# Kernel optimization log

Hardware: AMD Instinct MI355X
Metric: run time of the kernel (lower is better)

The kernel has to match this reference:

```python
import jax, jax.numpy as jnp
import numpy as np
import math

N_HEADS = 16
DIM = 1024
D_HEAD = DIM // N_HEADS
BS, QLEN = 2, 2048


def setup_inputs() -> dict:
    key = jax.random.key(0)
    ks = jax.random.split(key, 10)
    s = 0.02
    return {
        "input": jax.random.normal(ks[0], (BS, QLEN, DIM), dtype=jnp.float32),
        "mask": jnp.ones((BS, QLEN), dtype=jnp.int32),
        "q_w": jax.random.normal(ks[1], (DIM, DIM), dtype=jnp.float32) * s,
        "q_b": jax.random.normal(ks[2], (DIM,), dtype=jnp.float32) * s,
        "k_w": jax.random.normal(ks[3], (DIM, DIM), dtype=jnp.float32) * s,
        "k_b": jax.random.normal(ks[4], (DIM,), dtype=jnp.float32) * s,
        "v_w": jax.random.normal(ks[5], (DIM, DIM), dtype=jnp.float32) * s,
        "v_b": jax.random.normal(ks[6], (DIM,), dtype=jnp.float32) * s,
        "o_w": jax.random.normal(ks[7], (DIM, DIM), dtype=jnp.float32) * s,
        "o_b": jax.random.normal(ks[8], (DIM,), dtype=jnp.float32) * s,
    }


def _shape(x, bs):
    # (bs, len, dim) -> (bs, heads, len, d_head)
    return x.reshape(bs, -1, N_HEADS, D_HEAD).transpose(0, 2, 1, 3)


def reference(input, mask, q_w, q_b, k_w, k_b, v_w, v_b, o_w, o_b):
    bs, qlen, dim = input.shape
    # projections (torch Linear: x @ W^T + b)
    q = _shape(input @ q_w.T + q_b, bs)
    k = _shape(input @ k_w.T + k_b, bs)
    v = _shape(input @ v_w.T + v_b, bs)
    q = q / math.sqrt(D_HEAD)
    # scores: (bs, heads, qlen, klen)
    scores = jnp.einsum("bhqd,bhkd->bhqk", q, k)
    pad = (mask == 0)[:, None, None, :]  # (bs,1,1,klen)
    scores = jnp.where(pad, -jnp.inf, scores)
    weights = jax.nn.softmax(scores.astype(jnp.float32), axis=-1).astype(scores.dtype)
    # dropout p=0.0 (eval) -> identity
    context = jnp.einsum("bhqk,bhkd->bhqd", weights, v)
    context = context.transpose(0, 2, 1, 3).reshape(bs, qlen, dim)
    return context @ o_w.T + o_b
```

## Files before the change

kernel.cpp:

```cpp
#include <hip/hip_runtime.h>


#define BS    2
#define QLEN  2048
#define DIM   1024
#define NH    16
#define DH    64
#define MTOK  (BS * QLEN)

#define QSCALE 0.18033688011112042f

typedef __attribute__((ext_vector_type(8))) short short8;
typedef __attribute__((ext_vector_type(4))) float float4_t;
typedef __attribute__((ext_vector_type(4))) int   int4_t;

__device__ __forceinline__ ushort f2bf(float f) {
    unsigned u = __float_as_uint(f);
    return (ushort)((u + 0x7fffu + ((u >> 16) & 1u)) >> 16);
}
__device__ __forceinline__ short8 pack8(float4 a0, float4 a1) {
    short8 r;
    r[0] = (short)f2bf(a0.x); r[1] = (short)f2bf(a0.y);
    r[2] = (short)f2bf(a0.z); r[3] = (short)f2bf(a0.w);
    r[4] = (short)f2bf(a1.x); r[5] = (short)f2bf(a1.y);
    r[6] = (short)f2bf(a1.z); r[7] = (short)f2bf(a1.w);
    return r;
}

__device__ __forceinline__ void glds16(const void* g, void* l) {
    __builtin_amdgcn_global_load_lds(
        (const __attribute__((address_space(1))) unsigned int*)g,
        (__attribute__((address_space(3))) unsigned int*)l, 16, 0, 0);
}

__global__ __launch_bounds__(256) void conv_all(
    const float* __restrict__ x,  const float* __restrict__ qw,
    const float* __restrict__ kw, const float* __restrict__ vw,
    const float* __restrict__ ow,
    ushort* __restrict__ Xbf, ushort* __restrict__ Wbf)
{
    const int blk = blockIdx.x;
    const float* s; ushort* d; size_t base;
    if (blk < 4096)      { s = x;  d = Xbf;             base = (size_t)blk * 1024; }
    else if (blk < 5120) { s = qw; d = Wbf;             base = (size_t)(blk - 4096) * 1024; }
    else if (blk < 6144) { s = kw; d = Wbf + 1048576;   base = (size_t)(blk - 5120) * 1024; }
    else if (blk < 7168) { s = vw; d = Wbf + 2097152;   base = (size_t)(blk - 6144) * 1024; }
    else                 { s = ow; d = Wbf + 3145728;   base = (size_t)(blk - 7168) * 1024; }
    const size_t i = base + threadIdx.x * 4;
    float4 v = *(const float4*)(s + i);
    ushort4 o;
    o.x = f2bf(v.x); o.y = f2bf(v.y); o.z = f2bf(v.z); o.w = f2bf(v.w);
    *(ushort4*)(d + i) = o;
}

__global__ __launch_bounds__(256) void transpose_v(
    const ushort* __restrict__ Vrow, ushort* __restrict__ Vt)
{
    __shared__ ushort T[64][72];
    const int tid  = threadIdx.x;
    const int tile = blockIdx.x;
    const int bh   = blockIdx.y;
    const int b = bh >> 4, h = bh & 15;

    #pragma unroll
    for (int rep = 0; rep < 2; ++rep) {
        int ch = tid + rep * 256;
        int tok = ch >> 3, seg = ch & 7;
        uint4 v = *(const uint4*)(Vrow + (size_t)(b * QLEN + tile * 64 + tok) * DIM
                                        + h * DH + seg * 8);
        *(uint4*)&T[tok][seg * 8] = v;
    }
    __syncthreads();
    #pragma unroll
    for (int rep = 0; rep < 2; ++rep) {
        int ch = tid + rep * 256;
        int dim = ch >> 3, tseg = ch & 7;
        ushort t0 = T[tseg * 8 + 0][dim], t1 = T[tseg * 8 + 1][dim];
        ushort t2 = T[tseg * 8 + 2][dim], t3 = T[tseg * 8 + 3][dim];
        ushort t4 = T[tseg * 8 + 4][dim], t5 = T[tseg * 8 + 5][dim];
        ushort t6 = T[tseg * 8 + 6][dim], t7 = T[tseg * 8 + 7][dim];
        uint4 o;
        o.x = (unsigned)t0 | ((unsigned)t1 << 16);
        o.y = (unsigned)t2 | ((unsigned)t3 << 16);
        o.z = (unsigned)t4 | ((unsigned)t5 << 16);
        o.w = (unsigned)t6 | ((unsigned)t7 << 16);
        *(uint4*)(Vt + (size_t)bh * DH * QLEN + (size_t)dim * QLEN
                      + tile * 64 + tseg * 8) = o;
    }
}

__global__ __launch_bounds__(256) void gemm_qkv(
    const ushort* __restrict__ A, const ushort* __restrict__ Bw,
    const float* __restrict__ bias0, const float* __restrict__ bias1,
    const float* __restrict__ bias2,
    ushort* __restrict__ outQ, ushort* __restrict__ outK, ushort* __restrict__ outVt)
{
    __shared__ ushort As[2][128 * 32];
    __shared__ ushort Bs[2][128 * 32];
    const int tid  = threadIdx.x;
    const int w    = tid >> 6;
    const int lane = tid & 63;
    const int r15  = lane & 15;
    const int quad = lane >> 4;
    const int xcd = blockIdx.x & 7;
    const int lid = blockIdx.x >> 3;
    const int brow = (xcd & 3) * 8  + (lid & 7);
    const int bcol = (xcd >> 2) * 12 + (lid >> 3);
    const int wrow = (w >> 1) * 64;
    const int wcol = (w & 1) * 64;
    const int K = DIM;

    float4_t acc[4][4];
    #pragma unroll
    for (int i = 0; i < 4; ++i)
        #pragma unroll
        for (int j = 0; j < 4; ++j)
            acc[i][j] = (float4_t){0.f, 0.f, 0.f, 0.f};

    int chS[2];
    const ushort* gaS[2];
    const ushort* gbS[2];
    #pragma unroll
    for (int rep = 0; rep < 2; ++rep) {
        const int ch  = w * 128 + rep * 64 + lane;
        const int row = ch >> 2;
        const int g   = (ch & 3) ^ ((row >> 1) & 3);
        chS[rep] = ch;
        gaS[rep] = A  + (size_t)(brow * 128 + row) * K + g * 8;
        gbS[rep] = Bw + (size_t)(bcol * 128 + row) * K + g * 8;
    }
    const int ph = (quad ^ ((r15 >> 1) & 3)) * 8;

    #pragma unroll
    for (int rep = 0; rep < 2; ++rep) {
        glds16(gaS[rep], &As[0][chS[rep] * 8]);
        glds16(gbS[rep], &Bs[0][chS[rep] * 8]);
    }
    __syncthreads();

    int p = 0;
    for (int k0 = 0; k0 < K; k0 += 32) {
        if (k0 + 32 < K) {
            #pragma unroll
            for (int rep = 0; rep < 2; ++rep) {
                glds16(gaS[rep] + k0 + 32, &As[p ^ 1][chS[rep] * 8]);
                glds16(gbS[rep] + k0 + 32, &Bs[p ^ 1][chS[rep] * 8]);
            }
        }
        short8 af[4], bf[4];
        #pragma unroll
        for (int ms = 0; ms < 4; ++ms)
            af[ms] = *(const short8*)&As[p][(wrow + ms * 16 + r15) * 32 + ph];
        #pragma unroll
        for (int ns = 0; ns < 4; ++ns)
            bf[ns] = *(const short8*)&Bs[p][(wcol + ns * 16 + r15) * 32 + ph];
        #pragma unroll
        for (int ms = 0; ms < 4; ++ms)
            #pragma unroll
            for (int ns = 0; ns < 4; ++ns)
                acc[ms][ns] = __builtin_amdgcn_mfma_f32_16x16x32_bf16(
                    af[ms], bf[ns], acc[ms][ns], 0, 0, 0);
        __syncthreads();
        p ^= 1;
    }

    #pragma unroll
    for (int ms = 0; ms < 4; ++ms) {
        const int rowg = brow * 128 + wrow + ms * 16 + quad * 4;
        #pragma unroll
        for (int ns = 0; ns < 4; ++ns) {
            const int colg = bcol * 128 + wcol + ns * 16 + r15;
            if (colg < 1024) {
                const float bb = bias0[colg];
                #pragma unroll
                for (int r = 0; r < 4; ++r)
                    outQ[(size_t)(rowg + r) * 1024 + colg] =
                        f2bf((acc[ms][ns][r] + bb) * QSCALE);
            } else if (colg < 2048) {
                const float bb = bias1[colg - 1024];
                #pragma unroll
                for (int r = 0; r < 4; ++r)
                    outK[(size_t)(rowg + r) * 1024 + (colg - 1024)] =
                        f2bf(acc[ms][ns][r] + bb);
            } else {
                const int vcol = colg - 2048;
                const int hh = vcol >> 6, dd = vcol & 63;
                const float bb = bias2[vcol];
                const int bidx = rowg >> 11;
                const int tloc = rowg & 2047;
                ushort4 o4;
                o4.x = f2bf(acc[ms][ns][0] + bb);
                o4.y = f2bf(acc[ms][ns][1] + bb);
                o4.z = f2bf(acc[ms][ns][2] + bb);
                o4.w = f2bf(acc[ms][ns][3] + bb);
                *(ushort4*)&outVt[((size_t)(bidx * 16 + hh) * 64 + dd) * QLEN + tloc] = o4;
            }
        }
    }
}

__global__ __launch_bounds__(256) void gemm_o(
    const ushort* __restrict__ A, const ushort* __restrict__ Bw,
    const float* __restrict__ bias, float* __restrict__ Out)
{
    __shared__ ushort As[2][128 * 64];
    __shared__ ushort Bs[2][64 * 64];
    const int tid  = threadIdx.x;
    const int w    = tid >> 6;
    const int lane = tid & 63;
    const int r15  = lane & 15;
    const int quad = lane >> 4;
    const int xcd = blockIdx.x & 7;
    const int lid = blockIdx.x >> 3;
    const int brow = (xcd & 3) * 8 + (lid & 7);
    const int bcol = (xcd >> 2) * 8 + (lid >> 3);
    const int wrow = w * 32;
    const int K = DIM;

    float4_t acc[2][4];
    #pragma unroll
    for (int i = 0; i < 2; ++i)
        #pragma unroll
        for (int j = 0; j < 4; ++j)
            acc[i][j] = (float4_t){0.f, 0.f, 0.f, 0.f};

    int chA[4];  const ushort* gaS[4];
    #pragma unroll
    for (int rep = 0; rep < 4; ++rep) {
        const int ch  = w * 256 + rep * 64 + lane;
        const int row = ch >> 3;
        const int g   = (ch & 7) ^ (row & 7);
        chA[rep] = ch;
        gaS[rep] = A + (size_t)(brow * 128 + row) * K + g * 8;
    }
    int chB[2];  const ushort* gbS[2];
    #pragma unroll
    for (int rep = 0; rep < 2; ++rep) {
        const int ch  = w * 128 + rep * 64 + lane;
        const int row = ch >> 3;
        const int g   = (ch & 7) ^ (row & 7);
        chB[rep] = ch;
        gbS[rep] = Bw + (size_t)(bcol * 64 + row) * K + g * 8;
    }
    const int xg = r15 & 7;

    #pragma unroll
    for (int rep = 0; rep < 4; ++rep)
        glds16(gaS[rep], &As[0][chA[rep] * 8]);
    #pragma unroll
    for (int rep = 0; rep < 2; ++rep)
        glds16(gbS[rep], &Bs[0][chB[rep] * 8]);
    __syncthreads();

    int p = 0;
    for (int k0 = 0; k0 < K; k0 += 64) {
        if (k0 + 64 < K) {
            #pragma unroll
            for (int rep = 0; rep < 4; ++rep)
                glds16(gaS[rep] + k0 + 64, &As[p ^ 1][chA[rep] * 8]);
            #pragma unroll
            for (int rep = 0; rep < 2; ++rep)
                glds16(gbS[rep] + k0 + 64, &Bs[p ^ 1][chB[rep] * 8]);
        }
        #pragma unroll
        for (int hh = 0; hh < 2; ++hh) {
            const int ph = ((hh * 4 + quad) ^ xg) * 8;
            short8 af[2], bf[4];
            #pragma unroll
            for (int ms = 0; ms < 2; ++ms)
                af[ms] = *(const short8*)&As[p][(wrow + ms * 16 + r15) * 64 + ph];
            #pragma unroll
            for (int ns = 0; ns < 4; ++ns)
                bf[ns] = *(const short8*)&Bs[p][(ns * 16 + r15) * 64 + ph];
            #pragma unroll
            for (int ms = 0; ms < 2; ++ms)
                #pragma unroll
                for (int ns = 0; ns < 4; ++ns)
                    acc[ms][ns] = __builtin_amdgcn_mfma_f32_16x16x32_bf16(
                        af[ms], bf[ns], acc[ms][ns], 0, 0, 0);
        }
        __syncthreads();
        p ^= 1;
    }

    #pragma unroll
    for (int ms = 0; ms < 2; ++ms) {
        const int rowg = brow * 128 + wrow + ms * 16 + quad * 4;
        #pragma unroll
        for (int ns = 0; ns < 4; ++ns) {
            const int colg = bcol * 64 + ns * 16 + r15;
            const float bb = bias[colg];
            #pragma unroll
            for (int r = 0; r < 4; ++r)
                Out[(size_t)(rowg + r) * 1024 + colg] = acc[ms][ns][r] + bb;
        }
    }
}

__global__ __launch_bounds__(256) void gemm_f32in_bf16out(
    const float* __restrict__ X, const float* __restrict__ W,
    const float* __restrict__ B, ushort* __restrict__ Out,
    int M, int N, int K, float scale)
{
    const int lane = threadIdx.x & 63;
    const int wid  = (blockIdx.x * blockDim.x + threadIdx.x) >> 6;
    const int tilesN = N >> 4;
    const int tm = wid / tilesN;
    const int tn = wid - tm * tilesN;
    const int r15  = lane & 15;
    const int quad = lane >> 4;

    const float* xp = X + (size_t)(tm * 16 + r15) * K + quad * 8;
    const float* wp = W + (size_t)(tn * 16 + r15) * K + quad * 8;

    float4_t acc = {0.f, 0.f, 0.f, 0.f};
    for (int k0 = 0; k0 < K; k0 += 32) {
        float4 a0 = *(const float4*)(xp + k0);
        float4 a1 = *(const float4*)(xp + k0 + 4);
        float4 b0 = *(const float4*)(wp + k0);
        float4 b1 = *(const float4*)(wp + k0 + 4);
        acc = __builtin_amdgcn_mfma_f32_16x16x32_bf16(pack8(a0, a1), pack8(b0, b1), acc, 0, 0, 0);
    }
    const int col  = tn * 16 + r15;
    const float bias = B[col];
    const int row0 = tm * 16 + quad * 4;
    #pragma unroll
    for (int r = 0; r < 4; ++r)
        Out[(size_t)(row0 + r) * N + col] = f2bf((acc[r] + bias) * scale);
}

__global__ __launch_bounds__(256) void gemm_bf16in_f32out(
    const ushort* __restrict__ X, const float* __restrict__ W,
    const float* __restrict__ B, float* __restrict__ Out,
    int M, int N, int K)
{
    const int lane = threadIdx.x & 63;
    const int wid  = (blockIdx.x * blockDim.x + threadIdx.x) >> 6;
    const int tilesN = N >> 4;
    const int tm = wid / tilesN;
    const int tn = wid - tm * tilesN;
    const int r15  = lane & 15;
    const int quad = lane >> 4;

    const ushort* xp = X + (size_t)(tm * 16 + r15) * K + quad * 8;
    const float*  wp = W + (size_t)(tn * 16 + r15) * K + quad * 8;

    float4_t acc = {0.f, 0.f, 0.f, 0.f};
    for (int k0 = 0; k0 < K; k0 += 32) {
        short8 a = *(const short8*)(xp + k0);
        float4 b0 = *(const float4*)(wp + k0);
        float4 b1 = *(const float4*)(wp + k0 + 4);
        acc = __builtin_amdgcn_mfma_f32_16x16x32_bf16(a, pack8(b0, b1), acc, 0, 0, 0);
    }
    const int col  = tn * 16 + r15;
    const float bias = B[col];
    const int row0 = tm * 16 + quad * 4;
    #pragma unroll
    for (int r = 0; r < 4; ++r)
        Out[(size_t)(row0 + r) * N + col] = acc[r] + bias;
}

__global__ __launch_bounds__(256, 2) void flash_attn(
    const ushort* __restrict__ Qb, const ushort* __restrict__ Kb,
    const ushort* __restrict__ Vt, const int* __restrict__ mask,
    ushort* __restrict__ Cb)
{
    __shared__ __align__(16) ushort Ks[2][64][64];
    __shared__ __align__(16) ushort Vs[2][64][64];
    __shared__ __align__(16) float  Mb[QLEN];

    const int tid  = threadIdx.x;
    const int w    = tid >> 6;
    const int lane = tid & 63;
    const int r15  = lane & 15;
    const int quad = lane >> 4;
    const int bh = blockIdx.y;
    const int b = bh >> 4, h = bh & 15;

    {
        const int4* m4 = (const int4*)(mask + b * QLEN);
        #pragma unroll
        for (int rep = 0; rep < 2; ++rep) {
            const int idx = tid + rep * 256;
            int4 mv = m4[idx];
            float4 o;
            o.x = mv.x ? 0.f : -INFINITY;
            o.y = mv.y ? 0.f : -INFINITY;
            o.z = mv.z ? 0.f : -INFINITY;
            o.w = mv.w ? 0.f : -INFINITY;
            *(float4*)&Mb[idx * 4] = o;
        }
    }

    const int qbase = blockIdx.x * 128 + w * 32;
    const ushort* qp = Qb + (size_t)(b * QLEN + qbase + r15) * DIM + h * DH + quad * 8;
    short8 qf[2][2];
    qf[0][0] = *(const short8*)(qp);
    qf[0][1] = *(const short8*)(qp + 32);
    qf[1][0] = *(const short8*)(qp + 16 * DIM);
    qf[1][1] = *(const short8*)(qp + 16 * DIM + 32);

    const ushort* kg = Kb + (size_t)b * QLEN * DIM + h * DH;
    const ushort* vg = Vt + (size_t)bh * DH * QLEN;

    int cc0, cc1;
    const ushort* gk[2];
    const ushort* gv[2];
    {
        #pragma unroll
        for (int rep = 0; rep < 2; ++rep) {
            const int c   = (w * 2 + rep) * 64 + lane;
            const int row = c >> 3, slot = c & 7;
            const int sg  = slot ^ (row & 7);
            const int r5  = row & 31;
            const int tok = (row & 32) | (((r5 >> 3) & 1) << 4) | (((r5 >> 2) & 1) << 3)
                          | (((r5 >> 4) & 1) << 2) | (r5 & 3);
            if (rep == 0) cc0 = c; else cc1 = c;
            gk[rep] = kg + (size_t)tok * DIM  + sg * 8;
            gv[rep] = vg + (size_t)row * QLEN + sg * 8;
        }
    }

    const int xq = (quad ^ (r15 & 7)) << 3;

    float4_t o[2][4];
    float4_t ol[2];
    #pragma unroll
    for (int rg = 0; rg < 2; ++rg) {
        ol[rg] = (float4_t){0.f, 0.f, 0.f, 0.f};
        #pragma unroll
        for (int ds = 0; ds < 4; ++ds)
            o[rg][ds] = (float4_t){0.f, 0.f, 0.f, 0.f};
    }
    short8 ones8;
    #pragma unroll
    for (int i = 0; i < 8; ++i) ones8[i] = (short)0x3F80;

    int pkA[4][2][2], pkB[4][2][2];

#define STAGE_K(BUF, KT) do {                                                 \
    glds16(gk[0] + (size_t)(KT) * DIM, (ushort*)Ks[BUF] + cc0 * 8);           \
    glds16(gk[1] + (size_t)(KT) * DIM, (ushort*)Ks[BUF] + cc1 * 8);           \
} while (0)

#define STAGE_V(BUF, KT) do {                                                 \
    glds16(gv[0] + (KT), (ushort*)Vs[BUF] + cc0 * 8);                         \
    glds16(gv[1] + (KT), (ushort*)Vs[BUF] + cc1 * 8);                         \
} while (0)

#define S_PHASE(KBUF, KT, PK) do {                                            \
    _Pragma("unroll")                                                         \
    for (int ks = 0; ks < 4; ++ks) {                                          \
        const ushort* krow = &Ks[KBUF][ks * 16 + r15][0];                     \
        short8 kf0 = *(const short8*)(krow + xq);                             \
        short8 kf1 = *(const short8*)(krow + (xq ^ 32));                      \
        const float4 mb = *(const float4*)&Mb[(KT) + ((ks >> 1) << 5)         \
                                              + (quad << 3) + ((ks & 1) << 2)]; \
        _Pragma("unroll")                                                     \
        for (int rg = 0; rg < 2; ++rg) {                                      \
            float4_t s = {0.f, 0.f, 0.f, 0.f};                                \
            s = __builtin_amdgcn_mfma_f32_16x16x32_bf16(kf0, qf[rg][0], s, 0, 0, 0); \
            s = __builtin_amdgcn_mfma_f32_16x16x32_bf16(kf1, qf[rg][1], s, 0, 0, 0); \
            unsigned u0 = __float_as_uint(__builtin_amdgcn_exp2f(s[0] + mb.x)); \
            unsigned u1 = __float_as_uint(__builtin_amdgcn_exp2f(s[1] + mb.y)); \
            unsigned u2 = __float_as_uint(__builtin_amdgcn_exp2f(s[2] + mb.z)); \
            unsigned u3 = __float_as_uint(__builtin_amdgcn_exp2f(s[3] + mb.w)); \
            PK[ks][rg][0] = __builtin_amdgcn_perm(u1, u0, 0x07060302);        \
            PK[ks][rg][1] = __builtin_amdgcn_perm(u3, u2, 0x07060302);        \
        }                                                                     \
    }                                                                         \
} while (0)

#define PV_PHASE(VBUF, PK) do {                                               \
    __builtin_amdgcn_s_setprio(1);                                            \
    _Pragma("unroll")                                                         \
    for (int ck = 0; ck < 2; ++ck) {                                          \
        short8 vf[4];                                                         \
        _Pragma("unroll")                                                     \
        for (int ds = 0; ds < 4; ++ds)                                        \
            vf[ds] = *(const short8*)(&Vs[VBUF][ds * 16 + r15][0] + (xq ^ (ck << 5))); \
        _Pragma("unroll")                                                     \
        for (int rg = 0; rg < 2; ++rg) {                                      \
            int4_t pfi = { PK[2 * ck][rg][0], PK[2 * ck][rg][1],              \
                           PK[2 * ck + 1][rg][0], PK[2 * ck + 1][rg][1] };    \
            short8 pf = __builtin_bit_cast(short8, pfi);                      \
            _Pragma("unroll")                                                 \
            for (int ds = 0; ds < 4; ++ds)                                    \
                o[rg][ds] = __builtin_amdgcn_mfma_f32_16x16x32_bf16(          \
                    pf, vf[ds], o[rg][ds], 0, 0, 0);                          \
            ol[rg] = __builtin_amdgcn_mfma_f32_16x16x32_bf16(                 \
                pf, ones8, ol[rg], 0, 0, 0);                                  \
        }                                                                     \
    }                                                                         \
    __builtin_amdgcn_s_setprio(0);                                            \
} while (0)

    STAGE_K(0, 0); STAGE_V(0, 0); STAGE_K(1, 64);
    __syncthreads();
    S_PHASE(0, 0, pkA);
    __syncthreads();

    for (int kb = 0; kb < 1856; kb += 128) {
        STAGE_V(1, kb + 64); STAGE_K(0, kb + 128);
        S_PHASE(1, kb + 64, pkB);
        PV_PHASE(0, pkA);
        __syncthreads();
        STAGE_V(0, kb + 128); STAGE_K(1, kb + 192);
        S_PHASE(0, kb + 128, pkA);
        PV_PHASE(1, pkB);
        __syncthreads();
    }

    STAGE_V(1, 1984);
    S_PHASE(1, 1984, pkB);
    PV_PHASE(0, pkA);
    __syncthreads();
    PV_PHASE(1, pkB);

#undef STAGE_K
#undef STAGE_V
#undef S_PHASE
#undef PV_PHASE

    #pragma unroll
    for (int rg = 0; rg < 2; ++rg) {
        #pragma unroll
        for (int r = 0; r < 4; ++r) {
            const float ir = 1.f / fmaxf(ol[rg][r], 1e-30f);
            const size_t rb = (size_t)(b * QLEN + qbase + rg * 16 + quad * 4 + r) * DIM
                              + h * DH;
            Cb[rb +  0 + r15] = f2bf(o[rg][0][r] * ir);
            Cb[rb + 16 + r15] = f2bf(o[rg][1][r] * ir);
            Cb[rb + 32 + r15] = f2bf(o[rg][2][r] * ir);
            Cb[rb + 48 + r15] = f2bf(o[rg][3][r] * ir);
        }
    }
}

extern "C" void kernel_launch(void* const* d_in, const int* in_sizes, int n_in,
                              void* d_out, int out_size, void* d_ws, size_t ws_size,
                              hipStream_t stream)
{
    const float* x    = (const float*)d_in[0];
    const int*   mask = (const int*)d_in[1];
    const float* q_w  = (const float*)d_in[2];
    const float* q_b  = (const float*)d_in[3];
    const float* k_w  = (const float*)d_in[4];
    const float* k_b  = (const float*)d_in[5];
    const float* v_w  = (const float*)d_in[6];
    const float* v_b  = (const float*)d_in[7];
    const float* o_w  = (const float*)d_in[8];
    const float* o_b  = (const float*)d_in[9];
    float* out = (float*)d_out;

    const size_t SEG = (size_t)MTOK * DIM;
    ushort* Qbf = (ushort*)d_out;
    ushort* Xbf = Qbf + SEG;
    ushort* Kb  = (ushort*)d_ws;
    ushort* Cb  = Kb + SEG;
    ushort* Vt  = Cb + SEG;
    ushort* Wbf = Vt + SEG;

    const bool big = ws_size >= (size_t)32 * 1024 * 1024;

    if (big) {
        conv_all<<<8192, 256, 0, stream>>>(x, q_w, k_w, v_w, o_w, Xbf, Wbf);
        gemm_qkv<<<(MTOK / 128) * (3072 / 128), 256, 0, stream>>>(
            Xbf, Wbf, q_b, k_b, v_b, Qbf, Kb, Vt);
        flash_attn<<<dim3(QLEN / 128, BS * NH), 256, 0, stream>>>(Qbf, Kb, Vt, mask, Cb);
        gemm_o<<<(MTOK / 128) * (DIM / 64), 256, 0, stream>>>(
            Cb, Wbf + 3 * (size_t)(DIM * DIM), o_b, out);
    } else {
        const int tiles   = (MTOK / 16) * (DIM / 16);
        const int gblocks = tiles / 4;
        gemm_f32in_bf16out<<<gblocks, 256, 0, stream>>>(x, q_w, q_b, Qbf, MTOK, DIM, DIM, QSCALE);
        gemm_f32in_bf16out<<<gblocks, 256, 0, stream>>>(x, k_w, k_b, Kb,  MTOK, DIM, DIM, 1.0f);
        gemm_f32in_bf16out<<<gblocks, 256, 0, stream>>>(x, v_w, v_b, Cb,  MTOK, DIM, DIM, 1.0f);
        transpose_v<<<dim3(QLEN / 64, BS * NH), 256, 0, stream>>>(Cb, Vt);
        flash_attn<<<dim3(QLEN / 128, BS * NH), 256, 0, stream>>>(Qbf, Kb, Vt, mask, Cb);
        gemm_bf16in_f32out<<<tiles / 4, 256, 0, stream>>>(Cb, o_w, o_b, out, MTOK, DIM, DIM);
    }
}
```

Measured before the change: 193.4 us.

## Double K/V tile depth to 128 keys per stage and read mask from global

The flash-attention kernel now stages 128 keys per pipeline step instead of 64, which halves the number of __syncthreads barriers and loop iterations. The shared-memory mask buffer is removed; each S phase loads the int mask directly from global and folds it into the MFMA accumulator init. In exchange, LDS use doubles to about 64KB per block and the P-fragment registers double, which risks lower occupancy under launch_bounds(256,2) and more register pressure.

```diff
diff --git a/kernel.cpp b/kernel.cpp
--- a/kernel.cpp
+++ b/kernel.cpp
@@ -365,9 +365,8 @@
     const ushort* __restrict__ Vt, const int* __restrict__ mask,
     ushort* __restrict__ Cb)
 {
-    __shared__ __align__(16) ushort Ks[2][64][64];
-    __shared__ __align__(16) ushort Vs[2][64][64];
-    __shared__ __align__(16) float  Mb[QLEN];
+    __shared__ __align__(16) ushort Ks[2][2][64][64];
+    __shared__ __align__(16) ushort Vs[2][2][64][64];
 
     const int tid  = threadIdx.x;
     const int w    = tid >> 6;
@@ -377,21 +376,6 @@
     const int bh = blockIdx.y;
     const int b = bh >> 4, h = bh & 15;
 
-    {
-        const int4* m4 = (const int4*)(mask + b * QLEN);
-        #pragma unroll
-        for (int rep = 0; rep < 2; ++rep) {
-            const int idx = tid + rep * 256;
-            int4 mv = m4[idx];
-            float4 o;
-            o.x = mv.x ? 0.f : -INFINITY;
-            o.y = mv.y ? 0.f : -INFINITY;
-            o.z = mv.z ? 0.f : -INFINITY;
-            o.w = mv.w ? 0.f : -INFINITY;
-            *(float4*)&Mb[idx * 4] = o;
-        }
-    }
-
     const int qbase = blockIdx.x * 128 + w * 32;
     const ushort* qp = Qb + (size_t)(b * QLEN + qbase + r15) * DIM + h * DH + quad * 8;
     short8 qf[2][2];
@@ -402,23 +386,21 @@
 
     const ushort* kg = Kb + (size_t)b * QLEN * DIM + h * DH;
     const ushort* vg = Vt + (size_t)bh * DH * QLEN;
-
-    int cc0, cc1;
-    const ushort* gk[2];
-    const ushort* gv[2];
-    {
-        #pragma unroll
-        for (int rep = 0; rep < 2; ++rep) {
-            const int c   = (w * 2 + rep) * 64 + lane;
-            const int row = c >> 3, slot = c & 7;
-            const int sg  = slot ^ (row & 7);
-            const int r5  = row & 31;
-            const int tok = (row & 32) | (((r5 >> 3) & 1) << 4) | (((r5 >> 2) & 1) << 3)
-                          | (((r5 >> 4) & 1) << 2) | (r5 & 3);
-            if (rep == 0) cc0 = c; else cc1 = c;
-            gk[rep] = kg + (size_t)tok * DIM  + sg * 8;
-            gv[rep] = vg + (size_t)row * QLEN + sg * 8;
-        }
+    const int*    mg = mask + b * QLEN;
+
+    int kOff[4], vOff[4];
+    #pragma unroll
+    for (int rep = 0; rep < 4; ++rep) {
+        const int c    = rep * 256 + tid;
+        const int sub  = c >> 9;
+        const int r    = (c >> 3) & 63;
+        const int slot = c & 7;
+        const int sg   = slot ^ (r & 7);
+        const int r5   = r & 31;
+        const int tokl = (r & 32) | (((r5 >> 3) & 1) << 4) | (((r5 >> 2) & 1) << 3)
+                       | (((r5 >> 4) & 1) << 2) | (r5 & 3);
+        kOff[rep] = (sub * 64 + tokl) * DIM + sg * 8;
+        vOff[rep] = r * QLEN + sub * 64 + sg * 8;
     }
 
     const int xq = (quad ^ (r15 & 7)) << 3;
@@ -436,53 +418,68 @@
     #pragma unroll
     for (int i = 0; i < 8; ++i) ones8[i] = (short)0x3F80;
 
-    int pkA[4][2][2], pkB[4][2][2];
-
-#define STAGE_K(BUF, KT) do {                                                 \
-    glds16(gk[0] + (size_t)(KT) * DIM, (ushort*)Ks[BUF] + cc0 * 8);           \
-    glds16(gk[1] + (size_t)(KT) * DIM, (ushort*)Ks[BUF] + cc1 * 8);           \
+    int pkA[2][4][2][2], pkB[2][4][2][2];
+
+#define STAGE_K(BUF, BASE) do {                                               \
+    _Pragma("unroll")                                                         \
+    for (int rep = 0; rep < 4; ++rep)                                         \
+        glds16(kg + (size_t)(BASE) * DIM + kOff[rep],                         \
+               (ushort*)Ks[BUF] + (rep * 256 + tid) * 8);                     \
 } while (0)
 
-#define STAGE_V(BUF, KT) do {                                                 \
-    glds16(gv[0] + (KT), (ushort*)Vs[BUF] + cc0 * 8);                         \
-    glds16(gv[1] + (KT), (ushort*)Vs[BUF] + cc1 * 8);                         \
+#define STAGE_V(BUF, BASE) do {                                               \
+    _Pragma("unroll")                                                         \
+    for (int rep = 0; rep < 4; ++rep)                                         \
+        glds16(vg + (BASE) + vOff[rep],                                       \
+               (ushort*)Vs[BUF] + (rep * 256 + tid) * 8);                     \
 } while (0)
 
-#define S_PHASE(KBUF, KT, PK) do {                                            \
+#define S_PAIR(KBUF, BASE, PK) do {                                           \
     _Pragma("unroll")                                                         \
-    for (int ks = 0; ks < 4; ++ks) {                                          \
-        const ushort* krow = &Ks[KBUF][ks * 16 + r15][0];                     \
-        short8 kf0 = *(const short8*)(krow + xq);                             \
-        short8 kf1 = *(const short8*)(krow + (xq ^ 32));                      \
-        const float4 mb = *(const float4*)&Mb[(KT) + ((ks >> 1) << 5)         \
-                                              + (quad << 3) + ((ks & 1) << 2)]; \
+    for (int sub = 0; sub < 2; ++sub) {                                       \
         _Pragma("unroll")                                                     \
-        for (int rg = 0; rg < 2; ++rg) {                                      \
-            float4_t s = {0.f, 0.f, 0.f, 0.f};                                \
-            s = __builtin_amdgcn_mfma_f32_16x16x32_bf16(kf0, qf[rg][0], s, 0, 0, 0); \
-            s = __builtin_amdgcn_mfma_f32_16x16x32_bf16(kf1, qf[rg][1], s, 0, 0, 0); \
-            unsigned u0 = __float_as_uint(__builtin_amdgcn_exp2f(s[0] + mb.x)); \
-            unsigned u1 = __float_as_uint(__builtin_amdgcn_exp2f(s[1] + mb.y)); \
-            unsigned u2 = __float_as_uint(__builtin_amdgcn_exp2f(s[2] + mb.z)); \
-            unsigned u3 = __float_as_uint(__builtin_amdgcn_exp2f(s[3] + mb.w)); \
-            PK[ks][rg][0] = __builtin_amdgcn_perm(u1, u0, 0x07060302);        \
-            PK[ks][rg][1] = __builtin_amdgcn_perm(u3, u2, 0x07060302);        \
+        for (int ks = 0; ks < 4; ++ks) {                                      \
+            const ushort* krow = &Ks[KBUF][sub][ks * 16 + r15][0];            \
+            short8 kf0 = *(const short8*)(krow + xq);                         \
+            short8 kf1 = *(const short8*)(krow + (xq ^ 32));                  \
+            const int4 mv = *(const int4*)(mg + (BASE) + sub * 64             \
+                                           + ((ks >> 1) << 5) + (quad << 3)   \
+                                           + ((ks & 1) << 2));                \
+            float4_t si;                                                      \
+            si[0] = mv.x ? 0.f : -INFINITY;                                   \
+            si[1] = mv.y ? 0.f : -INFINITY;                                   \
+            si[2] = mv.z ? 0.f : -INFINITY;                                   \
+            si[3] = mv.w ? 0.f : -INFINITY;                                   \
+            _Pragma("unroll")                                                 \
+            for (int rg = 0; rg < 2; ++rg) {                                  \
+                float4_t s = si;                                              \
+                s = __builtin_amdgcn_mfma_f32_16x16x32_bf16(kf0, qf[rg][0], s, 0, 0, 0); \
+                s = __builtin_amdgcn_mfma_f32_16x16x32_bf16(kf1, qf[rg][1], s, 0, 0, 0); \
+                unsigned u0 = __float_as_uint(__builtin_amdgcn_exp2f(s[0]));  \
+                unsigned u1 = __float_as_uint(__builtin_amdgcn_exp2f(s[1]));  \
+                unsigned u2 = __float_as_uint(__builtin_amdgcn_exp2f(s[2]));  \
+                unsigned u3 = __float_as_uint(__builtin_amdgcn_exp2f(s[3]));  \
+                PK[sub][ks][rg][0] = __builtin_amdgcn_perm(u1, u0, 0x07060302); \
+                PK[sub][ks][rg][1] = __builtin_amdgcn_perm(u3, u2, 0x07060302); \
+            }                                                                 \
         }                                                                     \
     }                                                                         \
 } while (0)
 
-#define PV_PHASE(VBUF, PK) do {                                               \
+#define PV_PAIR(VBUF, PK) do {                                                \
     __builtin_amdgcn_s_setprio(1);                                            \
     _Pragma("unroll")                                                         \
-    for (int ck = 0; ck < 2; ++ck) {                                          \
+    for (int g = 0; g < 4; ++g) {                                             \
+        const int sub = g >> 1, ckl = g & 1;                                  \
         short8 vf[4];                                                         \
         _Pragma("unroll")                                                     \
         for (int ds = 0; ds < 4; ++ds)                                        \
-            vf[ds] = *(const short8*)(&Vs[VBUF][ds * 16 + r15][0] + (xq ^ (ck << 5))); \
+            vf[ds] = *(const short8*)(&Vs[VBUF][sub][ds * 16 + r15][0]        \
+                                      + (xq ^ (ckl << 5)));                   \
         _Pragma("unroll")                                                     \
         for (int rg = 0; rg < 2; ++rg) {                                      \
-            int4_t pfi = { PK[2 * ck][rg][0], PK[2 * ck][rg][1],              \
-                           PK[2 * ck + 1][rg][0], PK[2 * ck + 1][rg][1] };    \
+            int4_t pfi = { PK[sub][2 * ckl][rg][0], PK[sub][2 * ckl][rg][1],  \
+                           PK[sub][2 * ckl + 1][rg][0], PK[sub][2 * ckl + 1][rg][1] }; \
             short8 pf = __builtin_bit_cast(short8, pfi);                      \
             _Pragma("unroll")                                                 \
             for (int ds = 0; ds < 4; ++ds)                                    \
@@ -495,32 +492,32 @@
     __builtin_amdgcn_s_setprio(0);                                            \
 } while (0)
 
-    STAGE_K(0, 0); STAGE_V(0, 0); STAGE_K(1, 64);
+    STAGE_K(0, 0); STAGE_V(0, 0); STAGE_K(1, 128);
     __syncthreads();
-    S_PHASE(0, 0, pkA);
+    S_PAIR(0, 0, pkA);
     __syncthreads();
 
-    for (int kb = 0; kb < 1856; kb += 128) {
-        STAGE_V(1, kb + 64); STAGE_K(0, kb + 128);
-        S_PHASE(1, kb + 64, pkB);
-        PV_PHASE(0, pkA);
+    for (int kb = 0; kb < 1792; kb += 256) {
+        STAGE_V(1, kb + 128); STAGE_K(0, kb + 256);
+        S_PAIR(1, kb + 128, pkB);
+        PV_PAIR(0, pkA);
         __syncthreads();
-        STAGE_V(0, kb + 128); STAGE_K(1, kb + 192);
-        S_PHASE(0, kb + 128, pkA);
-        PV_PHASE(1, pkB);
+        STAGE_V(0, kb + 256); STAGE_K(1, kb + 384);
+        S_PAIR(0, kb + 256, pkA);
+        PV_PAIR(1, pkB);
         __syncthreads();
     }
 
-    STAGE_V(1, 1984);
-    S_PHASE(1, 1984, pkB);
-    PV_PHASE(0, pkA);
+    STAGE_V(1, 1920);
+    S_PAIR(1, 1920, pkB);
+    PV_PAIR(0, pkA);
     __syncthreads();
-    PV_PHASE(1, pkB);
+    PV_PAIR(1, pkB);
 
 #undef STAGE_K
 #undef STAGE_V
-#undef S_PHASE
-#undef PV_PHASE
+#undef S_PAIR
+#undef PV_PAIR
 
     #pragma unroll
     for (int rg = 0; rg < 2; ++rg) {
```

After: 191.8 us. About the same (-0.8%).
